# Kernel tuning notes

Hardware: AMD Instinct MI355X
Metric: run time of the kernel (lower is better)

## Reference

```python
import jax, jax.numpy as jnp
import numpy as np

NUM_HEADS = 8
DIM_HEAD = 64
SCALE = DIM_HEAD * NUM_HEADS  # q *= dim_head * num_heads, as in the source


def setup_inputs() -> dict:
    key = jax.random.key(0)
    k1, k2, k3, k4 = jax.random.split(key, 4)
    B, C, H, W = 8, 64, 32, 32
    x = jax.random.normal(k1, (B, C, H, W), dtype=jnp.float32)
    # 1x1 conv == matmul over channels; small init keeps post-scale logits sane
    w_qkv = jax.random.normal(k2, (3 * NUM_HEADS * DIM_HEAD, C), dtype=jnp.float32) * 0.02
    rel_h = jax.random.normal(k3, (2 * H - 1, DIM_HEAD), dtype=jnp.float32) * 0.02
    rel_w = jax.random.normal(k4, (2 * W - 1, DIM_HEAD), dtype=jnp.float32) * 0.02
    return {"x": x, "w_qkv": w_qkv, "rel_h": rel_h, "rel_w": rel_w}


def _rel_indices(H, W):
    # flattened 2D grid positions
    pos_y = np.repeat(np.arange(H), W)  # [HW]
    pos_x = np.tile(np.arange(W), H)    # [HW]
    rel_y = pos_y[None, :] - pos_y[:, None] + (H - 1)  # [HW, HW] in [0, 2H-2]
    rel_x = pos_x[None, :] - pos_x[:, None] + (W - 1)  # [HW, HW] in [0, 2W-2]
    return jnp.asarray(rel_y), jnp.asarray(rel_x)


def reference(x, w_qkv, rel_h, rel_w):
    B, C, H, W = x.shape
    n = H * W
    # 1x1 conv (bias=False) -> per-pixel matmul
    xf = x.reshape(B, C, n)                              # b c n
    qkv = jnp.einsum('oc,bcn->bon', w_qkv, xf)           # b (3 h d) n
    q, k, v = jnp.split(qkv, 3, axis=1)
    def to_heads(t):  # b (h d) n -> b h n d
        return t.reshape(B, NUM_HEADS, DIM_HEAD, n).transpose(0, 1, 3, 2)
    q, k, v = to_heads(q), to_heads(k), to_heads(v)
    q = q * SCALE  # scale applied before QK^T AND before pos bias (in-place in torch)

    sim = jnp.einsum('bhid,bhjd->bhij', q, k)            # [B, h, n, n]

    # relative position bias: q_i . rel_h[dy] + q_i . rel_w[dx]
    logits_h = jnp.einsum('bhid,rd->bhir', q, rel_h)     # [B, h, n, 2H-1]
    logits_w = jnp.einsum('bhid,rd->bhir', q, rel_w)     # [B, h, n, 2W-1]
    rel_y, rel_x = _rel_indices(H, W)                    # [n, n] each
    i_idx = jnp.arange(n)[:, None]                       # [n, 1]
    bias = logits_h[:, :, i_idx, rel_y] + logits_w[:, :, i_idx, rel_x]  # [B,h,n,n]

    attn = jax.nn.softmax(sim + bias, axis=-1)
    out = jnp.einsum('bhij,bhjd->bhid', attn, v)         # [B, h, n, d]
    out = out.transpose(0, 1, 3, 2).reshape(B, NUM_HEADS * DIM_HEAD, H, W)
    return out
```

## Files before the change

### kernel.cpp

```cpp
#include <hip/hip_runtime.h>
#include <hip/hip_bf16.h>
#include <hip/hip_fp16.h>

typedef _Float16 h8 __attribute__((ext_vector_type(8)));
typedef _Float16 h2 __attribute__((ext_vector_type(2)));
typedef unsigned short us8 __attribute__((ext_vector_type(8)));
typedef float f4 __attribute__((ext_vector_type(4)));

#define NH 8
#define DH 64
#define NPIX 1024
#define CIN 64
#define NBH 64
#define QSCALE (512.0f * 1.44269504f)
#define LOSCALE 2048.0f
#define INV_LOSCALE (1.0f / 2048.0f)
#define DTHR 12.0f

__device__ __forceinline__ void gload_lds16(const void* g, void* lds) {
  __builtin_amdgcn_global_load_lds(
      (const __attribute__((address_space(1))) void*)g,
      (__attribute__((address_space(3))) void*)lds, 16, 0, 0);
}

__device__ __forceinline__ float fexp2(float x) {
#if __has_builtin(__builtin_amdgcn_exp2f)
  return __builtin_amdgcn_exp2f(x);
#else
  return exp2f(x);
#endif
}

__device__ __forceinline__ unsigned pk16(float a, float b) {
  auto r = __builtin_amdgcn_cvt_pkrtz(a, b);
  union { decltype(r) h; unsigned u; } x;
  x.h = r;
  return x.u;
}

__device__ __forceinline__ f4 max4(f4 a, f4 b) {
  f4 r;
  r[0] = fmaxf(a[0], b[0]); r[1] = fmaxf(a[1], b[1]);
  r[2] = fmaxf(a[2], b[2]); r[3] = fmaxf(a[3], b[3]);
  return r;
}

__global__ __launch_bounds__(256) void qkv_mfma(
    const float* __restrict__ x, const float* __restrict__ wqkv,
    _Float16* __restrict__ Qh, _Float16* __restrict__ Ql,
    _Float16* __restrict__ Kh, _Float16* __restrict__ Kl,
    _Float16* __restrict__ Vv) {
  __shared__ __align__(16) char QS[49152];
  char* Wh = QS;
  char* Wl = QS + 16384;
  char* Xh = QS + 32768;
  char* Xl = QS + 40960;

  const int tid = threadIdx.x;
  const int lane = tid & 63;
  const int w = tid >> 6;
  const int c = lane & 15;
  const int g = lane >> 4;
  const int o0 = blockIdx.x * 128;
  const int p0 = blockIdx.y * 64;
  const int b = blockIdx.z;

  #pragma unroll
  for (int it = 0; it < 4; ++it) {
    int task = tid + it * 256;
    int oct = task & 7, o = task >> 3;
    const f4* wr = (const f4*)(wqkv + (size_t)(o0 + o) * CIN + oct * 8);
    f4 wa = wr[0], wb = wr[1];
    h8 hi, lo;
    #pragma unroll
    for (int e = 0; e < 8; ++e) {
      float v = e < 4 ? wa[e] : wb[e - 4];
      _Float16 h = (_Float16)v;
      hi[e] = h;
      lo[e] = (_Float16)((v - (float)h) * LOSCALE);
    }
    int byo = o * 128 + ((oct ^ (o & 7)) << 4);
    *(h8*)(Wh + byo) = hi;
    *(h8*)(Wl + byo) = lo;
  }
  #pragma unroll
  for (int it = 0; it < 16; ++it) {
    int idx = tid + it * 256;
    int p = idx & 63, cc = idx >> 6;
    float v = x[((size_t)b * CIN + cc) * NPIX + p0 + p];
    _Float16 h = (_Float16)v;
    _Float16 l = (_Float16)((v - (float)h) * LOSCALE);
    int byo = p * 128 + (((cc >> 3) ^ (p & 7)) << 4) + (cc & 7) * 2;
    *(_Float16*)(Xh + byo) = h;
    *(_Float16*)(Xl + byo) = l;
  }
  __syncthreads();

  f4 zf = {0.f, 0.f, 0.f, 0.f};
  f4 acc[2][4], cor[2][4];
  #pragma unroll
  for (int oi = 0; oi < 2; ++oi)
    #pragma unroll
    for (int pi = 0; pi < 4; ++pi) { acc[oi][pi] = zf; cor[oi][pi] = zf; }

  const int ob = w * 32;
  #pragma unroll
  for (int kh = 0; kh < 2; ++kh) {
    h8 ah[2], al[2], bh[4], bl[4];
    #pragma unroll
    for (int oi = 0; oi < 2; ++oi) {
      int orow = ob + ((c >> 2) << 3) + (c & 3) + oi * 4;
      int ch = (((kh * 4 + g) ^ (orow & 7)) << 4);
      ah[oi] = *(const h8*)(Wh + orow * 128 + ch);
      al[oi] = *(const h8*)(Wl + orow * 128 + ch);
    }
    #pragma unroll
    for (int pi = 0; pi < 4; ++pi) {
      int prow = pi * 16 + c;
      int ch = (((kh * 4 + g) ^ (prow & 7)) << 4);
      bh[pi] = *(const h8*)(Xh + prow * 128 + ch);
      bl[pi] = *(const h8*)(Xl + prow * 128 + ch);
    }
    __builtin_amdgcn_s_setprio(1);
    #pragma unroll
    for (int oi = 0; oi < 2; ++oi)
      #pragma unroll
      for (int pi = 0; pi < 4; ++pi) {
        acc[oi][pi] = __builtin_amdgcn_mfma_f32_16x16x32_f16(ah[oi], bh[pi], acc[oi][pi], 0, 0, 0);
        cor[oi][pi] = __builtin_amdgcn_mfma_f32_16x16x32_f16(ah[oi], bl[pi], cor[oi][pi], 0, 0, 0);
        cor[oi][pi] = __builtin_amdgcn_mfma_f32_16x16x32_f16(al[oi], bh[pi], cor[oi][pi], 0, 0, 0);
      }
    __builtin_amdgcn_s_setprio(0);
  }

  const int part = o0 >> 9;
  const float scl = part == 0 ? QSCALE : 1.0f;
  _Float16* dsth = part == 0 ? Qh : (part == 1 ? Kh : Vv);
  _Float16* dstl = part == 0 ? Ql : (part == 1 ? Kl : nullptr);
  #pragma unroll
  for (int pi = 0; pi < 4; ++pi) {
    int obase = o0 + ob + 8 * g;
    int h = (obase >> 6) & 7;
    int d = obase & 63;
    int p_abs = p0 + pi * 16 + c;
    size_t off = (((size_t)(b * NH + h)) * NPIX + p_abs) * DH + d;
    h8 hv, lv;
    #pragma unroll
    for (int oi = 0; oi < 2; ++oi)
      #pragma unroll
      for (int reg = 0; reg < 4; ++reg) {
        float v = (acc[oi][pi][reg] + cor[oi][pi][reg] * INV_LOSCALE) * scl;
        _Float16 hh = (_Float16)v;
        hv[oi * 4 + reg] = hh;
        lv[oi * 4 + reg] = (_Float16)((v - (float)hh) * LOSCALE);
      }
    *(h8*)(dsth + off) = hv;
    if (dstl) *(h8*)(dstl + off) = lv;
  }
}

__global__ __launch_bounds__(256, 2) void attn_mfma(
    const _Float16* __restrict__ Qh, const _Float16* __restrict__ Ql,
    const _Float16* __restrict__ Kh, const _Float16* __restrict__ Kl,
    const _Float16* __restrict__ V,
    const float* __restrict__ rel_h, const float* __restrict__ rel_w,
    float* __restrict__ out) {
  __shared__ __align__(16) char SMem[65536];
  char* SP = SMem + 49152;
  _Float16* LHc = (_Float16*)(SMem + 57344);
  _Float16* LWT = (_Float16*)(SMem + 32768);
  float* OT = (float*)SMem;

  const int tid = threadIdx.x;
  const int lane = tid & 63;
  const int w = tid >> 6;
  const int wu = __builtin_amdgcn_readfirstlane(w);
  const int c = lane & 15;
  const int g = lane >> 4;
  const int bx = blockIdx.x;
  const int bh = ((bx & 7) << 3) | ((bx >> 3) & 7);
  const int i0 = (bx >> 6) << 7;
  const int swz = (c & 7) << 4;

  const _Float16* Qhg = Qh + (size_t)bh * NPIX * DH;
  const _Float16* Qlg = Ql + (size_t)bh * NPIX * DH;
  const _Float16* Khg = Kh + (size_t)bh * NPIX * DH;
  const _Float16* Klg = Kl + (size_t)bh * NPIX * DH;
  const _Float16* Vg  = V  + (size_t)bh * NPIX * DH;

  const h8* Qr0h = (const h8*)(Qhg + (size_t)(i0 + w * 32 + c) * DH);
  const h8* Qr0l = (const h8*)(Qlg + (size_t)(i0 + w * 32 + c) * DH);
  const h8* Qr1h = (const h8*)(Qhg + (size_t)(i0 + w * 32 + 16 + c) * DH);
  const h8* Qr1l = (const h8*)(Qlg + (size_t)(i0 + w * 32 + 16 + c) * DH);
  h8 q0h[2] = {Qr0h[g], Qr0h[4 + g]};
  h8 q0l[2] = {Qr0l[g], Qr0l[4 + g]};
  h8 q1h[2] = {Qr1h[g], Qr1h[4 + g]};
  h8 q1l[2] = {Qr1l[g], Qr1l[4 + g]};

  const int s0i = wu * 128 + lane;
  const int s1i = s0i + 64;
  const int ko0 = (s0i >> 3) * 128 + (((s0i & 7) ^ ((s0i >> 3) & 7)) << 4);
  const int ko1 = (s1i >> 3) * 128 + (((s1i & 7) ^ ((s1i >> 3) & 7)) << 4);

  #pragma unroll
  for (int it = 0; it < 2; ++it) {
    int task = tid + it * 256;
    int oct = task & 7, s = task >> 3;
    int ss = s < 63 ? s : 62;
    const float* sh = rel_h + (size_t)ss * DH + oct * 8;
    const float* sw = rel_w + (size_t)ss * DH + oct * 8;
    h8 hh, ww;
    #pragma unroll
    for (int e = 0; e < 8; ++e) {
      hh[e] = (_Float16)sh[e];
      ww[e] = (_Float16)sw[e];
    }
    int byo = s * 128 + ((oct ^ (s & 7)) << 4);
    *(h8*)(SMem + byo) = hh;
    *(h8*)(SMem + 16384 + byo) = ww;
  }
  __syncthreads();

  const int yi = (i0 + w * 32) >> 5;
  f4 zf = {0.f, 0.f, 0.f, 0.f};
  #pragma unroll
  for (int rs = 0; rs < 2; ++rs) {
    f4 lhD[4], lwD[4], lhDc[4], lwDc[4];
    #pragma unroll
    for (int st = 0; st < 4; ++st) { lhD[st] = zf; lwD[st] = zf; lhDc[st] = zf; lwDc[st] = zf; }
    #pragma unroll
    for (int kh = 0; kh < 2; ++kh) {
      h8 bq = rs ? q1h[kh] : q0h[kh];
      h8 bl = rs ? q1l[kh] : q0l[kh];
      #pragma unroll
      for (int st = 0; st < 4; ++st) {
        int srow = st * 16 + c;
        int chb = srow * 128 + (((kh * 4 + g) ^ (srow & 7)) << 4);
        h8 ra = *(const h8*)(SMem + chb);
        h8 wa = *(const h8*)(SMem + 16384 + chb);
        lhD[st]  = __builtin_amdgcn_mfma_f32_16x16x32_f16(ra, bq, lhD[st], 0, 0, 0);
        lhDc[st] = __builtin_amdgcn_mfma_f32_16x16x32_f16(ra, bl, lhDc[st], 0, 0, 0);
        lwD[st]  = __builtin_amdgcn_mfma_f32_16x16x32_f16(wa, bq, lwD[st], 0, 0, 0);
        lwDc[st] = __builtin_amdgcn_mfma_f32_16x16x32_f16(wa, bl, lwDc[st], 0, 0, 0);
      }
    }
    int lrow = w * 32 + rs * 16 + c;
    #pragma unroll
    for (int st = 0; st < 4; ++st)
      #pragma unroll
      for (int reg = 0; reg < 4; ++reg) {
        int s = st * 16 + 4 * g + reg;
        float lhv = lhD[st][reg] + lhDc[st][reg] * INV_LOSCALE;
        float lwv = lwD[st][reg] + lwDc[st][reg] * INV_LOSCALE;
        int k = s - 31 + yi;
        if (k >= 0 && k < 32) LHc[lrow * 32 + k] = (_Float16)lhv;
        LWT[lrow * 64 + s] = (_Float16)lwv;
      }
  }
  __syncthreads();

  h8 lwp0, lwp1;
  #pragma unroll
  for (int jbp = 0; jbp < 2; ++jbp)
    #pragma unroll
    for (int reg = 0; reg < 4; ++reg) {
      lwp0[jbp * 4 + reg] = LWT[(w * 32 + c) * 64 + 31 + jbp * 16 + 4 * g + reg - c];
      lwp1[jbp * 4 + reg] = LWT[(w * 32 + 16 + c) * 64 + 31 + jbp * 16 + 4 * g + reg - 16 - c];
    }
  __syncthreads();

  {
    gload_lds16((const char*)Khg + ko0, SMem + wu * 2048);
    gload_lds16((const char*)Khg + ko1, SMem + wu * 2048 + 1024);
    gload_lds16((const char*)Klg + ko0, SMem + 16384 + wu * 2048);
    gload_lds16((const char*)Klg + ko1, SMem + 16384 + wu * 2048 + 1024);
    int jp = tid & 31, dd = tid >> 5;
    const h8* vr = (const h8*)(Vg + (size_t)(2 * jp) * DH);
    h8 v0 = vr[dd], v1 = vr[8 + dd];
    us8 u0 = *(const us8*)&v0, u1 = *(const us8*)&v1;
    #pragma unroll
    for (int e = 0; e < 8; ++e) {
      int d = dd * 8 + e;
      unsigned int val = (unsigned int)u0[e] | ((unsigned int)u1[e] << 16);
      *(unsigned int*)(SMem + 32768 + d * 128 + (((jp >> 2) ^ (d & 7)) << 4) + (jp & 3) * 4) = val;
    }
  }
  __syncthreads();

  float m0 = -1e30f, m1 = -1e30f, lp0 = 0.f, lp1 = 0.f;
  f4 o0_[4], o1_[4];
  #pragma unroll
  for (int dt = 0; dt < 4; ++dt) { o0_[dt] = zf; o1_[dt] = zf; }

  int cur = 0;
  #pragma unroll 1
  for (int t = 0; t < 16; ++t) {
    char* Kc  = SMem + cur * 8192;
    char* KLc = SMem + 16384 + cur * 8192;
    char* Vc  = SMem + 32768 + cur * 8192;
    const int nxt = cur ^ 1;
    const bool pre = t < 15;
    const int jp = tid & 31, dd = tid >> 5;
    h8 v0 = {}, v1 = {};
    if (pre) {
      const char* kg  = (const char*)Khg + (size_t)(t + 1) * 8192;
      const char* klg = (const char*)Klg + (size_t)(t + 1) * 8192;
      gload_lds16(kg + ko0, SMem + nxt * 8192 + wu * 2048);
      gload_lds16(kg + ko1, SMem + nxt * 8192 + wu * 2048 + 1024);
      gload_lds16(klg + ko0, SMem + 16384 + nxt * 8192 + wu * 2048);
      gload_lds16(klg + ko1, SMem + 16384 + nxt * 8192 + wu * 2048 + 1024);
      const h8* vr = (const h8*)(Vg + (size_t)((t + 1) * 64 + 2 * jp) * DH);
      v0 = vr[dd];
      v1 = vr[8 + dd];
    }

    f4 s0[4], c0[4], s1[4], c1[4];
    #pragma unroll
    for (int jb = 0; jb < 4; ++jb) { s0[jb] = zf; c0[jb] = zf; s1[jb] = zf; c1[jb] = zf; }
    #pragma unroll
    for (int kh = 0; kh < 2; ++kh) {
      h8 b0h = q0h[kh], b0l = q0l[kh], b1h = q1h[kh], b1l = q1l[kh];
      #pragma unroll
      for (int jb = 0; jb < 4; ++jb) {
        int jrow = jb * 16 + c;
        int chb = jrow * 128 + (((kh * 4 + g) ^ (c & 7)) << 4);
        h8 ah = *(const h8*)(Kc + chb);
        h8 al = *(const h8*)(KLc + chb);
        __builtin_amdgcn_s_setprio(1);
        s0[jb] = __builtin_amdgcn_mfma_f32_16x16x32_f16(ah, b0h, s0[jb], 0, 0, 0);
        c0[jb] = __builtin_amdgcn_mfma_f32_16x16x32_f16(al, b0h, c0[jb], 0, 0, 0);
        c0[jb] = __builtin_amdgcn_mfma_f32_16x16x32_f16(ah, b0l, c0[jb], 0, 0, 0);
        s1[jb] = __builtin_amdgcn_mfma_f32_16x16x32_f16(ah, b1h, s1[jb], 0, 0, 0);
        c1[jb] = __builtin_amdgcn_mfma_f32_16x16x32_f16(al, b1h, c1[jb], 0, 0, 0);
        c1[jb] = __builtin_amdgcn_mfma_f32_16x16x32_f16(ah, b1l, c1[jb], 0, 0, 0);
        __builtin_amdgcn_s_setprio(0);
      }
    }

    auto finish = [&](f4* s_, f4* c_, const h8& lwp, float& m_s, float& lp,
                      f4* o_, int rs) {
      h2 lhu = *(const h2*)(LHc + (w * 32 + rs * 16 + c) * 32 + 2 * t);
      float lh01[2] = {(float)lhu[0], (float)lhu[1]};
      #pragma unroll
      for (int jb = 0; jb < 4; ++jb)
        #pragma unroll
        for (int reg = 0; reg < 4; ++reg)
          s_[jb][reg] += c_[jb][reg] * INV_LOSCALE +
                         (float)lwp[(jb & 1) * 4 + reg] + lh01[jb >> 1];
      f4 ab = max4(s_[0], s_[1]);
      f4 cd = max4(s_[2], s_[3]);
      f4 ef = max4(ab, cd);
      float mx = fmaxf(fmaxf(ef[0], ef[1]), fmaxf(ef[2], ef[3]));
      mx = fmaxf(mx, __shfl_xor(mx, 16, 64));
      mx = fmaxf(mx, __shfl_xor(mx, 32, 64));
      bool sk = mx <= m_s + DTHR;
      if (!__all(sk)) {
        float mn = fmaxf(m_s, mx);
        float corr = fexp2(m_s - mn);
        m_s = mn;
        lp *= corr;
        #pragma unroll
        for (int dt = 0; dt < 4; ++dt)
          #pragma unroll
          for (int reg = 0; reg < 4; ++reg)
            o_[dt][reg] *= corr;
      }
      float sum = 0.f;
      char* pbse = SP + w * 2048 + c * 128;
      #pragma unroll
      for (int jb = 0; jb < 4; ++jb) {
        f4 p;
        #pragma unroll
        for (int reg = 0; reg < 4; ++reg) {
          p[reg] = fexp2(s_[jb][reg] - m_s);
          sum += p[reg];
        }
        *(unsigned*)(pbse + ((jb * 32 + 8 * g) ^ swz)) = pk16(p[0], p[1]);
        *(unsigned*)(pbse + ((jb * 32 + 8 * g + 4) ^ swz)) = pk16(p[2], p[3]);
      }
      lp += sum;
    };

    finish(s0, c0, lwp0, m0, lp0, o0_, 0);
    __builtin_amdgcn_wave_barrier();

    h8 vbr[2][4];
    #pragma unroll
    for (int kh = 0; kh < 2; ++kh) {
      int och = ((kh * 4 + g) ^ (c & 7)) << 4;
      h8 pb = *(const h8*)(SP + w * 2048 + c * 128 + och);
      __builtin_amdgcn_s_setprio(1);
      #pragma unroll
      for (int dt = 0; dt < 4; ++dt) {
        vbr[kh][dt] = *(const h8*)(Vc + (dt * 16 + c) * 128 + och);
        o0_[dt] = __builtin_amdgcn_mfma_f32_16x16x32_f16(vbr[kh][dt], pb, o0_[dt], 0, 0, 0);
      }
      __builtin_amdgcn_s_setprio(0);
    }
    __builtin_amdgcn_wave_barrier();

    finish(s1, c1, lwp1, m1, lp1, o1_, 1);
    __builtin_amdgcn_wave_barrier();

    #pragma unroll
    for (int kh = 0; kh < 2; ++kh) {
      int och = ((kh * 4 + g) ^ (c & 7)) << 4;
      h8 pb = *(const h8*)(SP + w * 2048 + c * 128 + och);
      __builtin_amdgcn_s_setprio(1);
      #pragma unroll
      for (int dt = 0; dt < 4; ++dt)
        o1_[dt] = __builtin_amdgcn_mfma_f32_16x16x32_f16(vbr[kh][dt], pb, o1_[dt], 0, 0, 0);
      __builtin_amdgcn_s_setprio(0);
    }

    if (pre) {
      us8 u0 = *(const us8*)&v0, u1 = *(const us8*)&v1;
      char* Vn = SMem + 32768 + nxt * 8192;
      #pragma unroll
      for (int e = 0; e < 8; ++e) {
        int d = dd * 8 + e;
        unsigned int val = (unsigned int)u0[e] | ((unsigned int)u1[e] << 16);
        *(unsigned int*)(Vn + d * 128 + (((jp >> 2) ^ (d & 7)) << 4) + (jp & 3) * 4) = val;
      }
    }
    __syncthreads();
    cur = nxt;
  }

  float a0 = lp0;
  a0 += __shfl_xor(a0, 16, 64);
  a0 += __shfl_xor(a0, 32, 64);
  float r0 = __builtin_amdgcn_rcpf(a0);
  float a1 = lp1;
  a1 += __shfl_xor(a1, 16, 64);
  a1 += __shfl_xor(a1, 32, 64);
  float r1 = __builtin_amdgcn_rcpf(a1);
  #pragma unroll
  for (int dt = 0; dt < 4; ++dt)
    #pragma unroll
    for (int reg = 0; reg < 4; ++reg) {
      int d = dt * 16 + 4 * g + reg;
      int sw = (d & 7) << 3;
      int il0 = w * 32 + c;
      OT[d * 128 + (il0 ^ sw)] = o0_[dt][reg] * r0;
      OT[d * 128 + ((il0 + 16) ^ sw)] = o1_[dt][reg] * r1;
    }
  __syncthreads();
  #pragma unroll
  for (int it = 0; it < 8; ++it) {
    int task = tid + it * 256;
    int rq = task & 31, d = task >> 5;
    f4 vv = *(const f4*)&OT[d * 128 + ((rq * 4) ^ ((d & 7) << 3))];
    *(f4*)(out + (((size_t)bh * 64 + d) << 10) + i0 + rq * 4) = vv;
  }
}

extern "C" void kernel_launch(void* const* d_in, const int* in_sizes, int n_in,
                              void* d_out, int out_size, void* d_ws, size_t ws_size,
                              hipStream_t stream) {
  const float* x  = (const float*)d_in[0];
  const float* wq = (const float*)d_in[1];
  const float* rh = (const float*)d_in[2];
  const float* rw = (const float*)d_in[3];
  float* out = (float*)d_out;

  const size_t sz = (size_t)NBH * NPIX * DH;
  _Float16* Qh = (_Float16*)d_ws;
  _Float16* Ql = Qh + sz;
  _Float16* Kh = Ql + sz;
  _Float16* Kl = Kh + sz;
  _Float16* V  = Kl + sz;

  qkv_mfma<<<dim3(12, 16, 8), 256, 0, stream>>>(x, wq, Qh, Ql, Kh, Kl, V);
  attn_mfma<<<dim3(512), 256, 0, stream>>>(Qh, Ql, Kh, Kl, V, rh, rw, out);
}
```

Before: 79.86 us.

## Vectorize x staging, transpose LHc layout, widen P stores, drop a wave barrier

The x-to-LDS conversion in the QKV projection now uses float4 global loads and writes packed pairs of fp16 values, where before it did one scalar load and store per element. The LHc relative-height logits buffer is transposed to be indexed by k first, which changes the LDS access pattern in the softmax finish step. The two 32-bit stores of packed P probabilities are merged into one 64-bit store, and one wave barrier between the first PV MMA and the second finish is removed. Together these aim to cut LDS and global instruction count. Dropping the barrier relies on the second finish not overwriting the SP buffer before the earlier reads complete, and the LHc reads become two scalar fp16 loads instead of one h2 load.

```diff
diff --git a/kernel.cpp b/kernel.cpp
--- a/kernel.cpp
+++ b/kernel.cpp
@@ -83,16 +83,30 @@
     *(h8*)(Wh + byo) = hi;
     *(h8*)(Wl + byo) = lo;
   }
-  #pragma unroll
-  for (int it = 0; it < 16; ++it) {
-    int idx = tid + it * 256;
-    int p = idx & 63, cc = idx >> 6;
-    float v = x[((size_t)b * CIN + cc) * NPIX + p0 + p];
-    _Float16 h = (_Float16)v;
-    _Float16 l = (_Float16)((v - (float)h) * LOSCALE);
-    int byo = p * 128 + (((cc >> 3) ^ (p & 7)) << 4) + (cc & 7) * 2;
-    *(_Float16*)(Xh + byo) = h;
-    *(_Float16*)(Xl + byo) = l;
+  {
+    int kp = tid & 31;
+    int pgrp = tid >> 5;
+    const float* xr0 = x + ((size_t)b * CIN + 2 * kp) * NPIX + p0 + pgrp * 8;
+    const float* xr1 = xr0 + NPIX;
+    f4 a0 = *(const f4*)xr0, a1 = *(const f4*)(xr0 + 4);
+    f4 b0 = *(const f4*)xr1, b1 = *(const f4*)(xr1 + 4);
+    int oct = kp >> 2;
+    int slot4 = (kp & 3) * 4;
+    #pragma unroll
+    for (int e = 0; e < 8; ++e) {
+      float v0 = e < 4 ? a0[e] : a1[e - 4];
+      float v1 = e < 4 ? b0[e] : b1[e - 4];
+      _Float16 h0 = (_Float16)v0, h1 = (_Float16)v1;
+      float l0f = (v0 - (float)h0) * LOSCALE;
+      float l1f = (v1 - (float)h1) * LOSCALE;
+      int p = pgrp * 8 + e;
+      int byo = p * 128 + ((oct ^ (p & 7)) << 4) + slot4;
+      union { h2 h; unsigned u; } uh, ul;
+      uh.h[0] = h0; uh.h[1] = h1;
+      ul.h[0] = (_Float16)l0f; ul.h[1] = (_Float16)l1f;
+      *(unsigned*)(Xh + byo) = uh.u;
+      *(unsigned*)(Xl + byo) = ul.u;
+    }
   }
   __syncthreads();
 
@@ -253,7 +267,7 @@
         float lhv = lhD[st][reg] + lhDc[st][reg] * INV_LOSCALE;
         float lwv = lwD[st][reg] + lwDc[st][reg] * INV_LOSCALE;
         int k = s - 31 + yi;
-        if (k >= 0 && k < 32) LHc[lrow * 32 + k] = (_Float16)lhv;
+        if (k >= 0 && k < 32) LHc[k * 128 + lrow] = (_Float16)lhv;
         LWT[lrow * 64 + s] = (_Float16)lwv;
       }
   }
@@ -339,8 +353,9 @@
 
     auto finish = [&](f4* s_, f4* c_, const h8& lwp, float& m_s, float& lp,
                       f4* o_, int rs) {
-      h2 lhu = *(const h2*)(LHc + (w * 32 + rs * 16 + c) * 32 + 2 * t);
-      float lh01[2] = {(float)lhu[0], (float)lhu[1]};
+      int rr = w * 32 + rs * 16 + c;
+      float lh01[2] = {(float)LHc[(2 * t) * 128 + rr],
+                       (float)LHc[(2 * t + 1) * 128 + rr]};
       #pragma unroll
       for (int jb = 0; jb < 4; ++jb)
         #pragma unroll
@@ -375,8 +390,9 @@
           p[reg] = fexp2(s_[jb][reg] - m_s);
           sum += p[reg];
         }
-        *(unsigned*)(pbse + ((jb * 32 + 8 * g) ^ swz)) = pk16(p[0], p[1]);
-        *(unsigned*)(pbse + ((jb * 32 + 8 * g + 4) ^ swz)) = pk16(p[2], p[3]);
+        unsigned long long u = (unsigned long long)pk16(p[0], p[1]) |
+                               ((unsigned long long)pk16(p[2], p[3]) << 32);
+        *(unsigned long long*)(pbse + ((jb * 32 + 8 * g) ^ swz)) = u;
       }
       lp += sum;
     };
@@ -397,7 +413,6 @@
       }
       __builtin_amdgcn_s_setprio(0);
     }
-    __builtin_amdgcn_wave_barrier();
 
     finish(s1, c1, lwp1, m1, lp1, o1_, 1);
     __builtin_amdgcn_wave_barrier();
```

After: 77.92 us. 2.4% less time.
